# Performance work log

Measured on AMD Instinct MI355X. Metric: run time of the kernel, lower is better.

## Reference

```python
import jax, jax.numpy as jnp
import numpy as np

N_HEAD = 16
N_EMBD = 1024
CHUNK = 64
ROPE_BASE = 10000.0


def setup_inputs() -> dict:
    key = jax.random.key(0)
    k1, k2, k3 = jax.random.split(key, 3)
    B, T, C = 4, 4096, N_EMBD
    x = jax.random.normal(k1, (B, T, C), dtype=jnp.float32)
    # torch nn.Linear weights: (out_features, in_features), init-scale ~ 1/sqrt(C)
    w_attn = jax.random.normal(k2, (3 * C, C), dtype=jnp.float32) / np.sqrt(C)
    w_proj = jax.random.normal(k3, (C, C), dtype=jnp.float32) / np.sqrt(C)
    return {"x": x, "w_attn": w_attn, "w_proj": w_proj}


def _rope_tables(head_dim, chunk_size, dtype):
    # positions restart every chunk (Rotary with chunk_size)
    inv_freq = 1.0 / (ROPE_BASE ** (jnp.arange(0, head_dim, 2, dtype=jnp.float32) / head_dim))
    t = jnp.arange(chunk_size, dtype=jnp.float32)
    freqs = jnp.outer(t, inv_freq)  # (chunk, d/2)
    return jnp.cos(freqs).astype(dtype), jnp.sin(freqs).astype(dtype)


def _apply_rope(x, cos, sin):
    # x: (B, nc, chunk, H, d); cos/sin: (chunk, d/2)
    d = x.shape[-1] // 2
    x1, x2 = x[..., :d], x[..., d:]
    c = cos[None, None, :, None, :]
    s = sin[None, None, :, None, :]
    return jnp.concatenate([x1 * c + x2 * s, -x1 * s + x2 * c], axis=-1)


def reference(x, w_attn, w_proj):
    B, T, C = x.shape
    H, cs = N_HEAD, CHUNK
    d = C // H
    nc = T // cs
    qkv = jnp.einsum('btc,fc->btf', x, w_attn)
    q, k, v = jnp.split(qkv, 3, axis=2)
    # reshape to (B, n_chunks, chunk, H, d) — chunks are independent
    q = q.reshape(B, nc, cs, H, d)
    k = k.reshape(B, nc, cs, H, d)
    v = v.reshape(B, nc, cs, H, d)
    cos, sin = _rope_tables(d, cs, x.dtype)
    q = _apply_rope(q, cos, sin)
    k = _apply_rope(k, cos, sin)
    scale = 1.0 / np.sqrt(d)
    scores = jnp.einsum('bnqhd,bnkhd->bnhqk', q, k) * scale  # (B,nc,H,cs,cs)
    p = jax.nn.softmax(scores, axis=-1)
    y = jnp.einsum('bnhqk,bnkhd->bnqhd', p, v)
    y = y.reshape(B, T, C)
    return jnp.einsum('btc,oc->bto', y, w_proj)
```

## Files before the change

### kernel.cpp

```cpp
#include <hip/hip_runtime.h>
#include <math.h>

typedef __attribute__((ext_vector_type(8))) short short8;
typedef __attribute__((ext_vector_type(4))) short s16x4;
typedef __attribute__((ext_vector_type(4))) float floatx4;

__device__ __forceinline__ float bits2f(short u) {
  unsigned int x = ((unsigned int)(unsigned short)u) << 16;
  return __builtin_bit_cast(float, x);
}
__device__ __forceinline__ short f2bits(float f) {
  unsigned int x = __builtin_bit_cast(unsigned int, f);
  x += 0x7FFFu + ((x >> 16) & 1u);
  return (short)(x >> 16);
}

__device__ __forceinline__ void gload_lds16(const short* g, short* l) {
  __builtin_amdgcn_global_load_lds((const __attribute__((address_space(1))) void*)g,
                                   (__attribute__((address_space(3))) void*)l, 16, 0, 0);
}

__global__ __launch_bounds__(256) void cvt_bf16(const float* __restrict__ in,
                                                short* __restrict__ out, long n8) {
  long i = (long)blockIdx.x * 256 + threadIdx.x;
  const long stride = (long)gridDim.x * 256;
  for (; i < n8; i += stride) {
    const floatx4* p = (const floatx4*)(in + i * 8);
    floatx4 v0 = p[0], v1 = p[1];
    short8 o;
#pragma unroll
    for (int e = 0; e < 4; e++) { o[e] = f2bits(v0[e]); o[e + 4] = f2bits(v1[e]); }
    *(short8*)(out + i * 8) = o;
  }
}

__global__ __launch_bounds__(256) void rope_table(float* __restrict__ tab) {
  int i = blockIdx.x * 256 + threadIdx.x;
  if (i >= 64 * 32) return;
  int t = i >> 5, j = i & 31;
  float inv = exp2f(-(float)j * 0.41524101186092030f);
  float ang = (float)t * inv;
  tab[i * 2]     = cosf(ang);
  tab[i * 2 + 1] = sinf(ang);
}

template <bool COUT_F32>
__global__ __launch_bounds__(256) void gemm_lds(const short* __restrict__ A,
                                                const short* __restrict__ B,
                                                void* __restrict__ C,
                                                int M, int N, int K) {
  __shared__ __attribute__((aligned(16))) short sA[128 * 32];
  __shared__ __attribute__((aligned(16))) short sB[128 * 32];

  const int tid  = threadIdx.x;
  const int lane = tid & 63;
  const int wave = tid >> 6;
  const int frow = lane & 15;
  const int quad = lane >> 4;

  const int nwg = gridDim.x;
  const int cpx = nwg >> 3;
  const int bid = blockIdx.x;
  const int swz = (bid & 7) * cpx + (bid >> 3);
  const int nbx = N >> 7;
  const int bx  = swz % nbx;
  const int by  = swz / nbx;

  const long m0 = (long)by * 128;
  const long n0 = (long)bx * 128;

  const int  c0    = tid;
  const long aoff  = (m0 + (c0 >> 2)) * (long)K + (c0 & 3) * 8;
  const long boff  = (n0 + (c0 >> 2)) * (long)K + (c0 & 3) * 8;
  const long rstep = 64L * K;

  floatx4 acc[4][4];
#pragma unroll
  for (int i = 0; i < 4; i++)
#pragma unroll
    for (int j = 0; j < 4; j++) acc[i][j] = (floatx4){0.f, 0.f, 0.f, 0.f};

  const int arow = (wave >> 1) * 64 + frow;
  const int brow = (wave &  1) * 64 + frow;

  for (int k0 = 0; k0 < K; k0 += 32) {
    __syncthreads();
    gload_lds16(A + aoff + k0,         sA + c0 * 8);
    gload_lds16(A + aoff + rstep + k0, sA + c0 * 8 + 2048);
    gload_lds16(B + boff + k0,         sB + c0 * 8);
    gload_lds16(B + boff + rstep + k0, sB + c0 * 8 + 2048);
    __syncthreads();

    short8 a[4], b[4];
#pragma unroll
    for (int i = 0; i < 4; i++) a[i] = *(const short8*)&sA[(arow + i * 16) * 32 + quad * 8];
#pragma unroll
    for (int i = 0; i < 4; i++) b[i] = *(const short8*)&sB[(brow + i * 16) * 32 + quad * 8];
#pragma unroll
    for (int mi = 0; mi < 4; mi++)
#pragma unroll
      for (int ni = 0; ni < 4; ni++)
        acc[mi][ni] = __builtin_amdgcn_mfma_f32_16x16x32_bf16(a[mi], b[ni], acc[mi][ni], 0, 0, 0);
  }

  const long mrow0 = m0 + (wave >> 1) * 64;
  const long ncol0 = n0 + (wave &  1) * 64;
#pragma unroll
  for (int mi = 0; mi < 4; mi++)
#pragma unroll
    for (int ni = 0; ni < 4; ni++) {
      long row0 = mrow0 + mi * 16 + quad * 4;
      long col  = ncol0 + ni * 16 + frow;
#pragma unroll
      for (int r = 0; r < 4; r++) {
        if constexpr (COUT_F32)
          ((float*)C)[(row0 + r) * (long)N + col] = acc[mi][ni][r];
        else
          ((short*)C)[(row0 + r) * (long)N + col] = f2bits(acc[mi][ni][r]);
      }
    }
}

__global__ __launch_bounds__(64, 1) void attn_mfma(const short* __restrict__ qkv,
                                                   short* __restrict__ y,
                                                   const float* __restrict__ cstab) {
  const int lane = threadIdx.x;
  const int frow = lane & 15;
  const int quad = lane >> 4;
  const int h = blockIdx.x, chunk = blockIdx.y, b = blockIdx.z;
  const long rowbase = (long)b * 4096 + (long)chunk * 64;

  __shared__ __attribute__((aligned(16))) short vt[64][68];
  __shared__ __attribute__((aligned(16))) short ps[64][68];

  const short* qb = qkv + rowbase * 3072 + h * 64;

  short8 qf[4][2], kf[4][2];
#pragma unroll
  for (int i = 0; i < 4; i++) {
    const short* rq = qb + (long)(16 * i + frow) * 3072 + quad * 8;
    qf[i][0] = *(const short8*)(rq);
    qf[i][1] = *(const short8*)(rq + 32);
    kf[i][0] = *(const short8*)(rq + 1024);
    kf[i][1] = *(const short8*)(rq + 1056);
    const floatx4* tp = (const floatx4*)(cstab + ((16 * i + frow) * 32 + quad * 8) * 2);
    floatx4 tv0 = tp[0], tv1 = tp[1], tv2 = tp[2], tv3 = tp[3];
#define CS_(k) ((k) < 4 ? tv0[(k) & 3] : (k) < 8 ? tv1[(k) & 3] : (k) < 12 ? tv2[(k) & 3] : tv3[(k) & 3])
#pragma unroll
    for (int e = 0; e < 8; e++) {
      float c = CS_(2 * e), s = CS_(2 * e + 1);
      float a0 = bits2f(qf[i][0][e]), a1 = bits2f(qf[i][1][e]);
      qf[i][0][e] = f2bits(a0 * c + a1 * s);
      qf[i][1][e] = f2bits(a1 * c - a0 * s);
      float b0 = bits2f(kf[i][0][e]), b1 = bits2f(kf[i][1][e]);
      kf[i][0][e] = f2bits(b0 * c + b1 * s);
      kf[i][1][e] = f2bits(b1 * c - b0 * s);
    }
#undef CS_
  }

  const short* vb = qb + 2048 + (long)lane * 3072;
#pragma unroll
  for (int w = 0; w < 8; w++) {
    short8 v8 = *(const short8*)(vb + w * 8);
#pragma unroll
    for (int e = 0; e < 8; e++) vt[w * 8 + e][lane] = v8[e];
  }
  __syncthreads();

  floatx4 sc[4][4];
#pragma unroll
  for (int mi = 0; mi < 4; mi++)
#pragma unroll
    for (int ni = 0; ni < 4; ni++) {
      sc[mi][ni] = (floatx4){0.f, 0.f, 0.f, 0.f};
      sc[mi][ni] = __builtin_amdgcn_mfma_f32_16x16x32_bf16(qf[mi][0], kf[ni][0], sc[mi][ni], 0, 0, 0);
      sc[mi][ni] = __builtin_amdgcn_mfma_f32_16x16x32_bf16(qf[mi][1], kf[ni][1], sc[mi][ni], 0, 0, 0);
    }

  float is_[4][4];
#pragma unroll
  for (int mi = 0; mi < 4; mi++)
#pragma unroll
    for (int r = 0; r < 4; r++) {
      float mx = fmaxf(fmaxf(sc[mi][0][r], sc[mi][1][r]), fmaxf(sc[mi][2][r], sc[mi][3][r]));
      mx = fmaxf(mx, __shfl_xor(mx, 1));
      mx = fmaxf(mx, __shfl_xor(mx, 2));
      mx = fmaxf(mx, __shfl_xor(mx, 4));
      mx = fmaxf(mx, __shfl_xor(mx, 8));
      float sm = 0.f;
#pragma unroll
      for (int ni = 0; ni < 4; ni++) {
        float e_ = __expf((sc[mi][ni][r] - mx) * 0.125f);
        sc[mi][ni][r] = e_;
        sm += e_;
      }
      sm += __shfl_xor(sm, 1);
      sm += __shfl_xor(sm, 2);
      sm += __shfl_xor(sm, 4);
      sm += __shfl_xor(sm, 8);
      is_[mi][r] = 1.0f / sm;
    }

#pragma unroll
  for (int mi = 0; mi < 4; mi++)
#pragma unroll
    for (int ni = 0; ni < 4; ni++)
#pragma unroll
      for (int r = 0; r < 4; r++)
        ps[mi * 16 + quad * 4 + r][ni * 16 + frow] = f2bits(sc[mi][ni][r] * is_[mi][r]);
  __syncthreads();

  short8 pf[4][2], vf[4][2];
#pragma unroll
  for (int i = 0; i < 4; i++)
#pragma unroll
    for (int ks = 0; ks < 2; ks++) {
      const short* pp = &ps[frow + 16 * i][quad * 8 + 32 * ks];
      s16x4 p0 = *(const s16x4*)pp, p1 = *(const s16x4*)(pp + 4);
      const short* vp = &vt[frow + 16 * i][quad * 8 + 32 * ks];
      s16x4 v0 = *(const s16x4*)vp, v1 = *(const s16x4*)(vp + 4);
#pragma unroll
      for (int e = 0; e < 4; e++) {
        pf[i][ks][e] = p0[e]; pf[i][ks][e + 4] = p1[e];
        vf[i][ks][e] = v0[e]; vf[i][ks][e + 4] = v1[e];
      }
    }

  floatx4 oc[4][4];
#pragma unroll
  for (int mi = 0; mi < 4; mi++)
#pragma unroll
    for (int ni = 0; ni < 4; ni++) {
      oc[mi][ni] = (floatx4){0.f, 0.f, 0.f, 0.f};
      oc[mi][ni] = __builtin_amdgcn_mfma_f32_16x16x32_bf16(pf[mi][0], vf[ni][0], oc[mi][ni], 0, 0, 0);
      oc[mi][ni] = __builtin_amdgcn_mfma_f32_16x16x32_bf16(pf[mi][1], vf[ni][1], oc[mi][ni], 0, 0, 0);
    }

  __syncthreads();
#pragma unroll
  for (int mi = 0; mi < 4; mi++)
#pragma unroll
    for (int ni = 0; ni < 4; ni++)
#pragma unroll
      for (int r = 0; r < 4; r++)
        ps[mi * 16 + quad * 4 + r][ni * 16 + frow] = f2bits(oc[mi][ni][r]);
  __syncthreads();

  short* dst = y + (rowbase + lane) * 1024 + h * 64;
#pragma unroll
  for (int w = 0; w < 8; w++) {
    const short* rp = &ps[lane][w * 8];
    s16x4 o0 = *(const s16x4*)rp, o1 = *(const s16x4*)(rp + 4);
    short8 o8;
#pragma unroll
    for (int e = 0; e < 4; e++) { o8[e] = o0[e]; o8[e + 4] = o1[e]; }
    *(short8*)(dst + w * 8) = o8;
  }
}

extern "C" void kernel_launch(void* const* d_in, const int* in_sizes, int n_in,
                              void* d_out, int out_size, void* d_ws, size_t ws_size,
                              hipStream_t stream) {
  (void)in_sizes; (void)n_in; (void)out_size; (void)ws_size;
  const float* x      = (const float*)d_in[0];
  const float* w_attn = (const float*)d_in[1];
  const float* w_proj = (const float*)d_in[2];
  float* out = (float*)d_out;

  short* qkv = (short*)d_ws;
  short* yb  = qkv + (size_t)16384 * 3072;
  short* wab = yb;
  short* wpb = qkv;
  short* xb  = (short*)d_out;
  float* tab = (float*)((char*)d_out + (size_t)32 * 1024 * 1024);

  cvt_bf16<<<dim3(2048), 256, 0, stream>>>(x,      xb,  (long)16384 * 1024 / 8);
  cvt_bf16<<<dim3(1024), 256, 0, stream>>>(w_attn, wab, (long)3072 * 1024 / 8);
  rope_table<<<dim3(8), 256, 0, stream>>>(tab);
  gemm_lds<false><<<dim3(3072), 256, 0, stream>>>(xb, wab, qkv, 16384, 3072, 1024);
  attn_mfma<<<dim3(16, 64, 4), 64, 0, stream>>>(qkv, yb, tab);
  cvt_bf16<<<dim3(512), 256, 0, stream>>>(w_proj, wpb, (long)1024 * 1024 / 8);
  gemm_lds<true><<<dim3(1024), 256, 0, stream>>>(yb, wpb, out, 16384, 1024, 1024);
}
```

Before: 351.0 us.

## Replace 128x128 GEMM with 256x256 tile, 4-stage LDS pipelined kernel

Both projection GEMMs now use a 512-thread kernel with 256x256 output tiles and a 4-buffer LDS ring. Global-to-LDS loads run three k-steps ahead, tracked with explicit vmcnt waits and raw barriers. Each step's B-tile loads are placed between two halves of the MFMA work, and s_setprio raises priority around the MFMAs. This aims to hide global memory latency and double per-block reuse, at the cost of 128KB of LDS per block, more registers, and fewer blocks for the smaller output projection (256 blocks).

After: 319.3 us. 9.0% less time.

```diff
diff --git a/kernel.cpp b/kernel.cpp
--- a/kernel.cpp
+++ b/kernel.cpp
@@ -45,16 +45,18 @@
 }
 
 template <bool COUT_F32>
-__global__ __launch_bounds__(256) void gemm_lds(const short* __restrict__ A,
-                                                const short* __restrict__ B,
-                                                void* __restrict__ C,
-                                                int M, int N, int K) {
-  __shared__ __attribute__((aligned(16))) short sA[128 * 32];
-  __shared__ __attribute__((aligned(16))) short sB[128 * 32];
-
-  const int tid  = threadIdx.x;
-  const int lane = tid & 63;
-  const int wave = tid >> 6;
+__global__ __launch_bounds__(512, 2) void gemm256(const short* __restrict__ A,
+                                                  const short* __restrict__ B,
+                                                  void* __restrict__ C,
+                                                  int M, int N, int K) {
+  (void)M;
+  __shared__ __attribute__((aligned(16))) short lds[65536];
+
+  const int t    = threadIdx.x;
+  const int lane = t & 63;
+  const int wave = t >> 6;
+  const int wm   = wave >> 2;
+  const int wn   = wave & 3;
   const int frow = lane & 15;
   const int quad = lane >> 4;
 
@@ -62,51 +64,94 @@
   const int cpx = nwg >> 3;
   const int bid = blockIdx.x;
   const int swz = (bid & 7) * cpx + (bid >> 3);
-  const int nbx = N >> 7;
+  const int nbx = N >> 8;
   const int bx  = swz % nbx;
   const int by  = swz / nbx;
-
-  const long m0 = (long)by * 128;
-  const long n0 = (long)bx * 128;
-
-  const int  c0    = tid;
-  const long aoff  = (m0 + (c0 >> 2)) * (long)K + (c0 & 3) * 8;
-  const long boff  = (n0 + (c0 >> 2)) * (long)K + (c0 & 3) * 8;
-  const long rstep = 64L * K;
-
-  floatx4 acc[4][4];
-#pragma unroll
-  for (int i = 0; i < 4; i++)
+  const long m0 = (long)by * 256;
+  const long n0 = (long)bx * 256;
+
+  const int NT = K >> 5;
+
+  const int  srow  = t >> 2;
+  const int  scol  = (t & 3) * 8;
+  const long aoff0 = (m0 + srow) * (long)K + scol;
+  const long aoff1 = aoff0 + 128L * K;
+  const long boff0 = (n0 + srow) * (long)K + scol;
+  const long boff1 = boff0 + 128L * K;
+  const int  t8    = t * 8;
+
+  floatx4 acc[8][4];
+#pragma unroll
+  for (int i = 0; i < 8; i++)
 #pragma unroll
     for (int j = 0; j < 4; j++) acc[i][j] = (floatx4){0.f, 0.f, 0.f, 0.f};
 
-  const int arow = (wave >> 1) * 64 + frow;
-  const int brow = (wave &  1) * 64 + frow;
-
-  for (int k0 = 0; k0 < K; k0 += 32) {
-    __syncthreads();
-    gload_lds16(A + aoff + k0,         sA + c0 * 8);
-    gload_lds16(A + aoff + rstep + k0, sA + c0 * 8 + 2048);
-    gload_lds16(B + boff + k0,         sB + c0 * 8);
-    gload_lds16(B + boff + rstep + k0, sB + c0 * 8 + 2048);
-    __syncthreads();
-
-    short8 a[4], b[4];
-#pragma unroll
-    for (int i = 0; i < 4; i++) a[i] = *(const short8*)&sA[(arow + i * 16) * 32 + quad * 8];
-#pragma unroll
-    for (int i = 0; i < 4; i++) b[i] = *(const short8*)&sB[(brow + i * 16) * 32 + quad * 8];
-#pragma unroll
-    for (int mi = 0; mi < 4; mi++)
-#pragma unroll
-      for (int ni = 0; ni < 4; ni++)
-        acc[mi][ni] = __builtin_amdgcn_mfma_f32_16x16x32_bf16(a[mi], b[ni], acc[mi][ni], 0, 0, 0);
-  }
-
-  const long mrow0 = m0 + (wave >> 1) * 64;
-  const long ncol0 = n0 + (wave &  1) * 64;
-#pragma unroll
-  for (int mi = 0; mi < 4; mi++)
+  for (int p = 0; p < 3; ++p) {
+    short* la = lds + p * 16384;
+    const long kk = (long)p * 32;
+    gload_lds16(A + aoff0 + kk, la + t8);
+    gload_lds16(A + aoff1 + kk, la + t8 + 4096);
+    gload_lds16(B + boff0 + kk, la + 8192 + t8);
+    gload_lds16(B + boff1 + kk, la + 8192 + t8 + 4096);
+  }
+
+#define GSTEP(KT, VMSTR, DO_STAGE)                                                     \
+  {                                                                                    \
+    const int kt_ = (KT);                                                              \
+    asm volatile("s_barrier" ::: "memory");     \
+    if (DO_STAGE) {                                                                    \
+      short* sa = lds + ((kt_ + 3) & 3) * 16384;                                       \
+      const long kk = (long)(kt_ + 3) * 32;                                            \
+      gload_lds16(A + aoff0 + kk, sa + t8);                                            \
+      gload_lds16(A + aoff1 + kk, sa + t8 + 4096);                                     \
+    }                                                                                  \
+    asm volatile("s_waitcnt " VMSTR ::: "memory");   \
+    asm volatile("s_barrier" ::: "memory");               \
+    {                                                                                  \
+      const short* la = lds + (kt_ & 3) * 16384;                                       \
+      const short* lb = la + 8192;                                                     \
+      short8 af[8], bf[4];                                                             \
+      _Pragma("unroll")                                                                \
+      for (int ni = 0; ni < 4; ni++)                                                   \
+        bf[ni] = *(const short8*)&lb[(wn * 64 + ni * 16 + frow) * 32 + quad * 8];      \
+      _Pragma("unroll")                                                                \
+      for (int mi = 0; mi < 8; mi++)                                                   \
+        af[mi] = *(const short8*)&la[(wm * 128 + mi * 16 + frow) * 32 + quad * 8];     \
+      __builtin_amdgcn_s_setprio(1);                                                   \
+      _Pragma("unroll")                                                                \
+      for (int mi = 0; mi < 4; mi++)                                                   \
+        _Pragma("unroll")                                                              \
+        for (int ni = 0; ni < 4; ni++)                                                 \
+          acc[mi][ni] =                                                                \
+              __builtin_amdgcn_mfma_f32_16x16x32_bf16(af[mi], bf[ni], acc[mi][ni], 0, 0, 0); \
+      __builtin_amdgcn_s_setprio(0);                                                   \
+      if (DO_STAGE) {                                                                  \
+        short* sb = lds + ((kt_ + 3) & 3) * 16384;                                     \
+        const long kk = (long)(kt_ + 3) * 32;                                          \
+        gload_lds16(B + boff0 + kk, sb + 8192 + t8);                                   \
+        gload_lds16(B + boff1 + kk, sb + 8192 + t8 + 4096);                            \
+      }                                                                                \
+      __builtin_amdgcn_s_setprio(1);                                                   \
+      _Pragma("unroll")                                                                \
+      for (int mi = 4; mi < 8; mi++)                                                   \
+        _Pragma("unroll")                                                              \
+        for (int ni = 0; ni < 4; ni++)                                                 \
+          acc[mi][ni] =                                                                \
+              __builtin_amdgcn_mfma_f32_16x16x32_bf16(af[mi], bf[ni], acc[mi][ni], 0, 0, 0); \
+      __builtin_amdgcn_s_setprio(0);                                                   \
+    }                                                                                  \
+  }
+
+  for (int kt = 0; kt <= NT - 4; ++kt) GSTEP(kt, "vmcnt(10)", true);
+  GSTEP(NT - 3, "vmcnt(8)", false);
+  GSTEP(NT - 2, "vmcnt(4)", false);
+  GSTEP(NT - 1, "vmcnt(0)", false);
+#undef GSTEP
+
+  const long mrow0 = m0 + wm * 128;
+  const long ncol0 = n0 + wn * 64;
+#pragma unroll
+  for (int mi = 0; mi < 8; mi++)
 #pragma unroll
     for (int ni = 0; ni < 4; ni++) {
       long row0 = mrow0 + mi * 16 + quad * 4;
@@ -278,8 +323,8 @@
   cvt_bf16<<<dim3(2048), 256, 0, stream>>>(x,      xb,  (long)16384 * 1024 / 8);
   cvt_bf16<<<dim3(1024), 256, 0, stream>>>(w_attn, wab, (long)3072 * 1024 / 8);
   rope_table<<<dim3(8), 256, 0, stream>>>(tab);
-  gemm_lds<false><<<dim3(3072), 256, 0, stream>>>(xb, wab, qkv, 16384, 3072, 1024);
+  gemm256<false><<<dim3(768), 512, 0, stream>>>(xb, wab, qkv, 16384, 3072, 1024);
   attn_mfma<<<dim3(16, 64, 4), 64, 0, stream>>>(qkv, yb, tab);
   cvt_bf16<<<dim3(512), 256, 0, stream>>>(w_proj, wpb, (long)1024 * 1024 / 8);
-  gemm_lds<true><<<dim3(1024), 256, 0, stream>>>(yb, wpb, out, 16384, 1024, 1024);
-}
+  gemm256<true><<<dim3(256), 512, 0, stream>>>(yb, wpb, out, 16384, 1024, 1024);
+}
```
